# Kernel tuning notes

Measured on AMD Instinct MI355X. Metric: run time of the kernel, lower is better.

Reference implementation:

```python
import jax, jax.numpy as jnp
import numpy as np

B, C, D, J = 8, 2048, 128, 128

def setup_inputs() -> dict:
    key = jax.random.key(0)
    ks = jax.random.split(key, 24)
    s = 0.02
    inp = {
        "operation_features": jax.random.normal(ks[0], (B, C, D), jnp.float32),
        "relations": jax.random.randint(ks[1], (B, C - 2, 2), 0, C, jnp.int64),
        "begins_idx": jax.random.randint(ks[2], (B, J), 0, C, jnp.int64),
        "ends_idx": jax.random.randint(ks[3], (B, J), 0, C, jnp.int64),
        "same_type_mask": (jax.random.uniform(ks[4], (B, C, C)) > 0.5).astype(jnp.float32),
        # BeginEndEncoder
        "W_begin": jax.random.normal(ks[5], (D, D), jnp.float32) * s,
        "b_begin": jnp.zeros((D,), jnp.float32),
        "W_end": jax.random.normal(ks[6], (D, D), jnp.float32) * s,
        "b_end": jnp.zeros((D,), jnp.float32),
        # OperationTimeRelationEncoder.mix: Linear(3D -> D)
        "W_mix3": jax.random.normal(ks[7], (3 * D, D), jnp.float32) * s,
        "b_mix3": jnp.zeros((D,), jnp.float32),
        # SelfAttention (hidden_dim = D)
        "W_qkv": jax.random.normal(ks[8], (D, 3 * D), jnp.float32) * s,
        "b_qkv": jnp.zeros((3 * D,), jnp.float32),
        "w_score": jax.random.normal(ks[9], (2 * D,), jnp.float32) * s,
        "b_score": jnp.zeros((), jnp.float32),
        "W_out": jax.random.normal(ks[10], (D, D), jnp.float32) * s,
        "b_out": jnp.zeros((D,), jnp.float32),
        # block mix: Linear(2D -> D)
        "W_mix2": jax.random.normal(ks[11], (2 * D, D), jnp.float32) * s,
        "b_mix2": jnp.zeros((D,), jnp.float32),
    }
    return inp

def _gather_ops(ops, idx):
    # ops: [B,C,D], idx: [B,M] -> [B,M,D]  (torch.gather along dim 1 with expanded index)
    Bb, _, Dd = ops.shape
    M = idx.shape[1]
    return jnp.take_along_axis(ops, jnp.broadcast_to(idx[:, :, None], (Bb, M, Dd)), axis=1)

def reference(operation_features, relations, begins_idx, ends_idx, same_type_mask,
              W_begin, b_begin, W_end, b_end, W_mix3, b_mix3,
              W_qkv, b_qkv, w_score, b_score, W_out, b_out, W_mix2, b_mix2):
    ops = operation_features
    Dd = ops.shape[-1]
    # --- OperationTimeRelationEncoder ---
    pred = _gather_ops(ops, relations[..., 0])      # [B,C-2,D]
    succ = _gather_ops(ops, relations[..., 1])      # [B,C-2,D]
    concated = jnp.concatenate([ops[:, :-2, :], pred, succ], axis=-1)  # [B,C-2,3D]
    mixed = concated @ W_mix3 + b_mix3              # [B,C-2,D]
    begin_f = _gather_ops(ops, begins_idx) @ W_begin + b_begin  # [B,J,D]
    end_f = _gather_ops(ops, ends_idx) @ W_end + b_end
    begin = jnp.mean(begin_f, axis=1)               # [B,D]
    end = jnp.mean(end_f, axis=1)
    seq = jnp.concatenate([mixed, begin[:, None, :], end[:, None, :]], axis=1)  # [B,C,D]
    # --- SelfAttention (GAT-style additive score, decomposed to avoid CxCx2h blowup) ---
    qkv = ops @ W_qkv + b_qkv                       # [B,C,3D]
    q, k, v = jnp.split(qkv, 3, axis=-1)
    sq = q @ w_score[:Dd]                           # [B,C]  q_i . w_q
    sk = k @ w_score[Dd:]                           # [B,C]  k_j . w_k
    scores = jax.nn.leaky_relu(sq[:, :, None] + sk[:, None, :] + b_score)  # [B,C,C]
    attn = jax.nn.softmax(scores * same_type_mask, axis=-1)                # multiplicative mask, as in torch
    weighted = jnp.einsum('bij,bjd->bid', attn, v)  # [B,C,D]
    same_type = weighted @ W_out + b_out            # [B,C,D]
    # --- final mix ---
    return jnp.concatenate([seq, same_type], axis=-1) @ W_mix2 + b_mix2  # [B,C,D]
```

## Files before the change

kernel.cpp:

```cpp
#include <hip/hip_runtime.h>
#include <cstddef>

typedef __bf16 bf16;
typedef __bf16 bf16x4 __attribute__((ext_vector_type(4)));
typedef __bf16 bf16x8 __attribute__((ext_vector_type(8)));
typedef float  f32x4  __attribute__((ext_vector_type(4)));

#define MFMA16(a, b, c) __builtin_amdgcn_mfma_f32_16x16x32_bf16((a), (b), (c), 0, 0, 0)

#define BB 8
#define CC 2048
#define DD 128
#define JJN 128

#define WS_PK    ((size_t)0)
#define WS_OPS16 ((size_t)8388608)
#define WS_SQF   ((size_t)12582912)
#define WS_SKF   ((size_t)12648448)
#define WS_G1T   ((size_t)12713984)
#define WS_G2T   ((size_t)12746752)
#define WS_G3T   ((size_t)12779520)
#define WS_WCT   ((size_t)12812288)
#define WS_GBT   ((size_t)12845056)
#define WS_GET   ((size_t)12877824)
#define WS_UQK   ((size_t)12910592)
#define WS_BBM   ((size_t)12911104)
#define WS_BBB   ((size_t)12911616)
#define WS_BBE   ((size_t)12912128)
#define WS_SC    ((size_t)12912640)
#define WS_WCN   ((size_t)12913152)
#define WS_GBN   ((size_t)12945920)
#define WS_GEN   ((size_t)12978688)
#define WS_MEANV ((size_t)17205760)

__global__ __launch_bounds__(256) void k_prepcast(
    const float* __restrict__ ops, bf16* __restrict__ ops16,
    const int* __restrict__ begins, const int* __restrict__ ends,
    const float* __restrict__ Wmix3, const float* __restrict__ Wmix2,
    const float* __restrict__ Wout,  const float* __restrict__ Wbegin,
    const float* __restrict__ Wend,  const float* __restrict__ Wqkv,
    const float* __restrict__ bqkv,  const float* __restrict__ wscore,
    const float* __restrict__ bscore,const float* __restrict__ bmix3,
    const float* __restrict__ bout,  const float* __restrict__ bmix2,
    const float* __restrict__ bbegin,const float* __restrict__ bend,
    bf16* __restrict__ G1T, bf16* __restrict__ G2T, bf16* __restrict__ G3T,
    bf16* __restrict__ WCT, bf16* __restrict__ GBT, bf16* __restrict__ GET,
    bf16* __restrict__ WCN, bf16* __restrict__ GBN, bf16* __restrict__ GEN,
    bf16* __restrict__ uqk, float* __restrict__ BBM, float* __restrict__ BBB,
    float* __restrict__ BBE, float* __restrict__ sc, float* __restrict__ MEANV)
{
    __shared__ bf16  LshT[128 * 132];
    __shared__ float Rsh[128 * 8];
    int wg = blockIdx.x;
    int t  = threadIdx.x;

    if (wg == 0) {
        for (int half = 0; half < 2; ++half) {
            #pragma unroll
            for (int pass = 0; pass < 16; ++pass) {
                int idx = pass * 256 + t;
                int d   = idx >> 5;
                int e0  = (idx & 31) * 4;
                f32x4 v = *(const f32x4*)(Wqkv + d*384 + half*128 + e0);
                #pragma unroll
                for (int jj = 0; jj < 4; ++jj)
                    LshT[(e0 + jj)*132 + d] = (bf16)v[jj];
            }
            if (t < 32) {
                f32x4 wv = *(const f32x4*)(wscore + half*128 + t*4);
                #pragma unroll
                for (int jj = 0; jj < 4; ++jj) Rsh[t*4 + jj] = wv[jj];
            }
            __syncthreads();
            if (t < 128) {
                float s = 0.f;
                for (int e = 0; e < 128; ++e)
                    s += (float)LshT[e*132 + t] * Rsh[e];
                uqk[half*128 + t] = (bf16)s;
            }
            __syncthreads();
        }
        float bm = 0.f, bb_ = 0.f, be_ = 0.f, bon = 0.f;
        for (int half = 0; half < 2; ++half) {
            #pragma unroll
            for (int pass = 0; pass < 16; ++pass) {
                int idx = pass * 256 + t;
                int f   = idx >> 5;
                int e0  = (idx & 31) * 4;
                f32x4 v = *(const f32x4*)(Wmix2 + (size_t)(half*128 + f)*128 + e0);
                #pragma unroll
                for (int jj = 0; jj < 4; ++jj)
                    LshT[f*132 + e0 + jj] = (bf16)v[jj];
            }
            if (t < 32) {
                if (half == 0) {
                    f32x4 v0 = *(const f32x4*)(bmix3  + t*4);
                    f32x4 v1 = *(const f32x4*)(bbegin + t*4);
                    f32x4 v2 = *(const f32x4*)(bend   + t*4);
                    #pragma unroll
                    for (int jj = 0; jj < 4; ++jj) {
                        Rsh[t*4 + jj]       = v0[jj];
                        Rsh[128 + t*4 + jj] = v1[jj];
                        Rsh[256 + t*4 + jj] = v2[jj];
                    }
                } else {
                    f32x4 v3 = *(const f32x4*)(bout + t*4);
                    #pragma unroll
                    for (int jj = 0; jj < 4; ++jj) Rsh[t*4 + jj] = v3[jj];
                }
            }
            __syncthreads();
            if (t < 128) {
                if (half == 0) {
                    for (int f = 0; f < 128; ++f) {
                        float wv = (float)LshT[f*132 + t];
                        bm  += Rsh[f]       * wv;
                        bb_ += Rsh[128 + f] * wv;
                        be_ += Rsh[256 + f] * wv;
                    }
                } else {
                    for (int f = 0; f < 128; ++f)
                        bon += Rsh[f] * (float)LshT[f*132 + t];
                }
            }
            __syncthreads();
        }
        if (t < 128) {
            float bm2 = bmix2[t];
            BBM[t] = bm  + bon + bm2;
            BBB[t] = bb_ + bon + bm2;
            BBE[t] = be_ + bon + bm2;
        }
        if (t >= 128) {
            int e2 = t - 128;
            Rsh[512 + e2] = bqkv[e2]       * wscore[e2];
            Rsh[640 + e2] = bqkv[128 + e2] * wscore[128 + e2];
        }
        __syncthreads();
        if (t == 0) {
            float cq = 0.f, ck = 0.f;
            for (int e2 = 0; e2 < 128; ++e2) {
                cq += Rsh[512 + e2];
                ck += Rsh[640 + e2];
            }
            sc[0] = cq + bscore[0];
            sc[1] = ck;
        }
        return;
    }
    if (wg <= 16) {
        int task = wg - 1;
        int b2 = task >> 1, which = task & 1;
        const int* idxp = which ? (ends + b2 * JJN) : (begins + b2 * JJN);
        int* ish = (int*)Rsh;
        if (t < JJN) ish[t] = idxp[t];
        __syncthreads();
        int d = t & 127, half = t >> 7;
        const float* opsb = ops + (size_t)b2 * CC * DD;
        float s = 0.f;
        #pragma unroll 8
        for (int j = 0; j < 64; ++j) {
            int r = ish[half * 64 + j];
            s += opsb[(size_t)r * DD + d];
        }
        float* fsh = Rsh + 256;
        fsh[half * 128 + d] = s;
        __syncthreads();
        if (t < 128)
            MEANV[task * 128 + t] = (fsh[t] + fsh[128 + t]) * (1.0f / (float)JJN);
        return;
    }
    if (wg <= 112) {
        int id  = wg - 17;
        int mat = id >> 4, sub = id & 15;
        const float* L; const float* R; bf16* O; bf16* O2;
        switch (mat) {
            case 0: L = Wmix3;           R = Wmix2;           O = G1T; O2 = nullptr; break;
            case 1: L = Wmix3 + 128*128; R = Wmix2;           O = G2T; O2 = nullptr; break;
            case 2: L = Wmix3 + 256*128; R = Wmix2;           O = G3T; O2 = nullptr; break;
            case 3: L = Wout;            R = Wmix2 + 128*128; O = WCT; O2 = WCN; break;
            case 4: L = Wbegin;          R = Wmix2;           O = GBT; O2 = GBN; break;
            default:L = Wend;            R = Wmix2;           O = GET; O2 = GEN; break;
        }
        int e0 = sub * 8;
        #pragma unroll
        for (int pass = 0; pass < 16; ++pass) {
            int idx = pass * 256 + t;
            int d   = idx >> 5;
            int f0  = (idx & 31) * 4;
            f32x4 v = *(const f32x4*)(L + d * 128 + f0);
            #pragma unroll
            for (int jj = 0; jj < 4; ++jj)
                LshT[(f0 + jj) * 132 + d] = (bf16)v[jj];
        }
        #pragma unroll
        for (int pass = 0; pass < 4; ++pass) {
            int idx = pass * 256 + t;
            int f   = idx >> 3;
            int ee  = idx & 7;
            Rsh[f * 8 + ee] = R[f * 128 + e0 + ee];
        }
        __syncthreads();
        int ee = t >> 5;
        int e  = e0 + ee;
        int d0 = (t & 31) * 4;
        float s[4] = {0.f, 0.f, 0.f, 0.f};
        for (int f = 0; f < 128; ++f) {
            bf16x4 lv = *(const bf16x4*)&LshT[f * 132 + d0];
            float rv = Rsh[f * 8 + ee];
            #pragma unroll
            for (int dd = 0; dd < 4; ++dd)
                s[dd] += (float)lv[dd] * rv;
        }
        #pragma unroll
        for (int dd = 0; dd < 4; ++dd) {
            O[e * 128 + d0 + dd] = (bf16)s[dd];
            if (O2) O2[(d0 + dd) * 128 + e] = (bf16)s[dd];
        }
        return;
    }
    size_t i = (size_t)(wg - 113) * 256 + t;
    f32x4 a = *(const f32x4*)(ops + i * 8);
    f32x4 b = *(const f32x4*)(ops + i * 8 + 4);
    bf16x8 o;
    #pragma unroll
    for (int e = 0; e < 4; ++e) { o[e] = (bf16)a[e]; o[4 + e] = (bf16)b[e]; }
    *(bf16x8*)(ops16 + i * 8) = o;
}

__global__ __launch_bounds__(256) void k_v(
    const bf16* __restrict__ ops16, const float* __restrict__ Wqkv,
    const float* __restrict__ bqkv, const bf16* __restrict__ uqk,
    const float* __restrict__ sc,
    bf16* __restrict__ PK, float* __restrict__ sqf, float* __restrict__ skf)
{
    __shared__ bf16 A[144 * 136];
    int b  = blockIdx.x >> 4;
    int jt = (blockIdx.x & 15) * 128;
    int t  = threadIdx.x;
    #pragma unroll
    for (int pass = 0; pass < 16; ++pass) {
        int idx = pass * 256 + t;
        int d   = idx >> 5;
        int n0  = (idx & 31) * 4;
        f32x4 v = *(const f32x4*)(Wqkv + d*384 + 256 + n0);
        #pragma unroll
        for (int jj = 0; jj < 4; ++jj)
            A[(n0 + jj)*136 + d] = (bf16)v[jj];
    }
    {
        int row = t >> 7, col = t & 127;
        A[(128 + row)*136 + col] = uqk[row*128 + col];
    }
    for (int idx = t; idx < 14*136; idx += 256)
        A[130*136 + idx] = (bf16)0.f;
    __syncthreads();

    int lane = t & 63, w = t >> 6;
    int m = lane & 15, q = lane >> 4;
    f32x4 acc[9][2];
    #pragma unroll
    for (int rb = 0; rb < 9; ++rb)
        #pragma unroll
        for (int cb = 0; cb < 2; ++cb)
            acc[rb][cb] = {0.f, 0.f, 0.f, 0.f};

    const bf16* opsb = ops16 + (size_t)b * CC * DD;
    #pragma unroll
    for (int kc = 0; kc < 4; ++kc) {
        bf16x8 bfr[2];
        #pragma unroll
        for (int cb = 0; cb < 2; ++cb) {
            int j = jt + w*32 + cb*16 + m;
            bfr[cb] = *(const bf16x8*)(opsb + (size_t)j*DD + kc*32 + q*8);
        }
        #pragma unroll
        for (int rb = 0; rb < 9; ++rb) {
            bf16x8 afr = *(const bf16x8*)&A[(rb*16 + m)*136 + kc*32 + q*8];
            acc[rb][0] = MFMA16(afr, bfr[0], acc[rb][0]);
            acc[rb][1] = MFMA16(afr, bfr[1], acc[rb][1]);
        }
    }
    float cqb = sc[0], ckv = sc[1];
    #pragma unroll
    for (int cb = 0; cb < 2; ++cb) {
        int j = jt + w*32 + cb*16 + m;
        if (q == 0) {
            sqf[b*CC + j] = acc[8][cb][0] + cqb;
            skf[b*CC + j] = acc[8][cb][1] + ckv;
        }
    }
    __syncthreads();
    bf16* pack = A;
    #pragma unroll
    for (int cb = 0; cb < 2; ++cb) {
        int qq_base = cb*2 + (m>>3);
        int e       = m & 7;
        #pragma unroll
        for (int rb = 0; rb < 8; ++rb) {
            #pragma unroll
            for (int r = 0; r < 4; ++r) {
                float v = acc[rb][cb][r] + bqkv[256 + rb*16 + q*4 + r];
                pack[w*4096 + rb*512 + qq_base*128 + (q*4+r)*8 + e] = (bf16)v;
            }
        }
    }
    __syncthreads();
    bf16* pkb = PK + (size_t)b * DD * CC + (size_t)jt * 128;
    #pragma unroll
    for (int pass = 0; pass < 8; ++pass) {
        int lidx = pass * 256 + t;
        *(uint4*)(pkb + (size_t)lidx * 8) = *(const uint4*)&pack[lidx * 8];
    }
}

struct MaskLd { f32x4 v[8]; };

__device__ __forceinline__ MaskLd stage_load(const float* __restrict__ mrow0,
                                             int st, int lane)
{
    MaskLd L;
    int rr0 = lane >> 4, cc = (lane & 15) * 4;
    const float* src = mrow0 + st * 64 + cc;
    #pragma unroll
    for (int k = 0; k < 8; ++k)
        L.v[k] = __builtin_nontemporal_load(
            (const f32x4*)(src + ((size_t)(rr0 + k * 4)) * CC));
    return L;
}

__device__ __forceinline__ void stage_write(const MaskLd& L, bf16* mb,
                                            int buf, int lane)
{
    int rr0 = lane >> 4, cc = (lane & 15) * 4;
    bf16* dst = mb + buf * 2816;
    #pragma unroll
    for (int k = 0; k < 8; ++k) {
        bf16x4 o;
        #pragma unroll
        for (int e = 0; e < 4; ++e) o[e] = (bf16)L.v[k][e];
        *(bf16x4*)(dst + (rr0 + k * 4) * 88 + cc) = o;
    }
}

__device__ __forceinline__ void load_vb(const bf16* __restrict__ pkb, int jc,
                                        int q, int m, bf16x8 vb[8])
{
    #pragma unroll
    for (int nb = 0; nb < 8; ++nb)
        vb[nb] = *(const bf16x8*)(pkb + ((size_t)(((jc*8 + nb)*4 + q)*16 + m)) * 8);
}

__device__ __forceinline__ void substep(const bf16* mb, const float* skb,
    int buf, int st, int sub, int tile, int q, int m, float sq,
    const bf16x8 vb[8], float& lsum, f32x4 acc[8])
{
    bf16x8 mk = *(const bf16x8*)(mb + buf * 2816 + (tile*16 + m) * 88
                                 + sub * 32 + q * 8);
    int jo = st * 64 + sub * 32 + q * 8;
    f32x4 s0 = *(const f32x4*)(skb + jo);
    f32x4 s1 = *(const f32x4*)(skb + jo + 4);
    float sks[8] = {s0[0], s0[1], s0[2], s0[3], s1[0], s1[1], s1[2], s1[3]};
    bf16x8 a;
    #pragma unroll
    for (int e = 0; e < 8; ++e) {
        float tv = sq + sks[e];
        float lr = fmaxf(tv, 0.01f * tv);
        float z  = lr * (float)mk[e];
        float p  = __expf(z);
        lsum += p;
        a[e] = (bf16)p;
    }
    #pragma unroll
    for (int nb = 0; nb < 8; ++nb)
        acc[nb] = MFMA16(a, vb[nb], acc[nb]);
}

__global__ __launch_bounds__(256) void k_attepi(
    const float* __restrict__ mask, const bf16* __restrict__ PK,
    const float* __restrict__ sqf, const float* __restrict__ skf,
    const bf16* __restrict__ ops16, const int* __restrict__ relations,
    const bf16* __restrict__ G1T, const bf16* __restrict__ G2T,
    const bf16* __restrict__ G3T, const bf16* __restrict__ WCT,
    const bf16* __restrict__ GBN, const bf16* __restrict__ GEN,
    const bf16* __restrict__ WCN,
    const float* __restrict__ BBM, const float* __restrict__ BBB,
    const float* __restrict__ BBE, const float* __restrict__ MEANV,
    float* __restrict__ out)
{
    __shared__ __align__(16) char smem[53248];
    int t    = threadIdx.x;
    int lane = t & 63, w = t >> 6;
    int b    = blockIdx.x & 7;
    int i0   = (blockIdx.x >> 3) << 5;
    int m = lane & 15, q = lane >> 4;

    bf16*  mbuf = (bf16*)(smem + w * 11264);
    float* skb  = (float*)(smem + 45056 + w * 2048);

    {
        const float* src = skf + b*CC + w*512;
        f32x4 v0 = *(const f32x4*)(src + lane*4);
        f32x4 v1 = *(const f32x4*)(src + 256 + lane*4);
        *(f32x4*)(skb + lane*4) = v0;
        *(f32x4*)(skb + 256 + lane*4) = v1;
    }
    float sq0 = sqf[b*CC + i0 + m];
    float sq1 = sqf[b*CC + i0 + 16 + m];
    const float* mrow0 = mask + ((size_t)(b*CC + i0))*CC + w*512;
    const bf16*  pkb   = PK + (size_t)b * DD * CC;
    int jc0 = w * 16;

    f32x4 acc0[8], acc1[8];
    #pragma unroll
    for (int nb = 0; nb < 8; ++nb) {
        acc0[nb] = {0.f, 0.f, 0.f, 0.f};
        acc1[nb] = {0.f, 0.f, 0.f, 0.f};
    }
    float lsum0 = 0.f, lsum1 = 0.f;

    {   MaskLd r0 = stage_load(mrow0, 0, lane);
        stage_write(r0, mbuf, 0, lane); }
    MaskLd r1 = stage_load(mrow0, 1, lane);
    MaskLd r2 = stage_load(mrow0, 2, lane);

    int buf = 0;
    for (int st = 0; st < 8; ++st) {
        #pragma unroll
        for (int sub = 0; sub < 2; ++sub) {
            bf16x8 vb[8];
            load_vb(pkb, jc0 + st*2 + sub, q, m, vb);
            substep(mbuf, skb, buf, st, sub, 0, q, m, sq0, vb, lsum0, acc0);
            substep(mbuf, skb, buf, st, sub, 1, q, m, sq1, vb, lsum1, acc1);
        }
        if (st + 1 < 8) stage_write(r1, mbuf, buf ^ 1, lane);
        r1 = r2;
        if (st + 3 < 8) r2 = stage_load(mrow0, st + 3, lane);
        buf ^= 1;
    }

    __syncthreads();
    float* Osh  = (float*)smem;
    float* Lsh  = (float*)(smem + 33792);
    bf16*  Obuf = (bf16*)(smem + 43520);
    #pragma unroll
    for (int tile = 0; tile < 2; ++tile) {
        float ls = tile ? lsum1 : lsum0;
        ls += __shfl_xor(ls, 16, 64);
        ls += __shfl_xor(ls, 32, 64);
        if (q == 0) Lsh[w * 16 + m] = ls;
        const f32x4* acc = tile ? acc1 : acc0;
        #pragma unroll
        for (int nb = 0; nb < 8; ++nb)
            #pragma unroll
            for (int r = 0; r < 4; ++r)
                Osh[(w * 16 + q * 4 + r) * 132 + nb * 16 + m] = acc[nb][r];
        __syncthreads();

        int r   = t >> 4;
        int c0e = (t & 15) * 8;
        float l = Lsh[r] + Lsh[16 + r] + Lsh[32 + r] + Lsh[48 + r];
        float inv = 1.0f / l;
        bf16x8 o;
        #pragma unroll
        for (int e = 0; e < 8; ++e) {
            float s = Osh[r * 132 + c0e + e] + Osh[(16 + r) * 132 + c0e + e]
                    + Osh[(32 + r) * 132 + c0e + e] + Osh[(48 + r) * 132 + c0e + e];
            o[e] = (bf16)(s * inv);
        }
        *(bf16x8*)&Obuf[(tile * 16 + r) * 136 + c0e] = o;
        __syncthreads();
    }

    bf16* Abuf = (bf16*)smem;
    bf16* Bbuf = (bf16*)(smem + 8704);

    f32x4 eacc[2][2];
    #pragma unroll
    for (int rb = 0; rb < 2; ++rb)
        #pragma unroll
        for (int cb = 0; cb < 2; ++cb)
            eacc[rb][cb] = {0.f, 0.f, 0.f, 0.f};

    const bf16* Bsrc[4] = {G1T, G2T, G3T, WCT};
    int arow = t >> 3, ao = (t & 7) * 16;
    int brow = t >> 1, bo2 = (t & 1) * 64;
    int c = i0 + arow;

    for (int term = 0; term < 4; ++term) {
        if (term < 3) {
            const bf16* src;
            if (term == 0) src = ops16 + ((size_t)(b * CC + c)) * DD;
            else {
                int ridx = relations[((size_t)b * (CC - 2) + min(c, CC - 3)) * 2 + (term - 1)];
                src = ops16 + ((size_t)(b * CC) + ridx) * DD;
            }
            *(uint4*)&Abuf[arow * 136 + ao]     = *(const uint4*)(src + ao);
            *(uint4*)&Abuf[arow * 136 + ao + 8] = *(const uint4*)(src + ao + 8);
        }
        const uint4* bs = (const uint4*)(Bsrc[term] + brow * 128 + bo2);
        uint4* bd = (uint4*)&Bbuf[brow * 136 + bo2];
        #pragma unroll
        for (int ii = 0; ii < 8; ++ii) bd[ii] = bs[ii];
        __syncthreads();

        const bf16* Asrc = (term == 3) ? Obuf : Abuf;
        #pragma unroll
        for (int kc = 0; kc < 4; ++kc) {
            bf16x8 bfr[2];
            #pragma unroll
            for (int cb = 0; cb < 2; ++cb)
                bfr[cb] = *(const bf16x8*)&Bbuf[(w * 32 + cb * 16 + m) * 136 + kc * 32 + q * 8];
            #pragma unroll
            for (int rb = 0; rb < 2; ++rb) {
                bf16x8 afr = *(const bf16x8*)&Asrc[(rb * 16 + m) * 136 + kc * 32 + q * 8];
                eacc[rb][0] = MFMA16(afr, bfr[0], eacc[rb][0]);
                eacc[rb][1] = MFMA16(afr, bfr[1], eacc[rb][1]);
            }
        }
        __syncthreads();
    }
    #pragma unroll
    for (int cb = 0; cb < 2; ++cb) {
        int col = w * 32 + cb * 16 + m;
        float bias = BBM[col];
        #pragma unroll
        for (int rb = 0; rb < 2; ++rb) {
            #pragma unroll
            for (int r = 0; r < 4; ++r) {
                int cg = i0 + rb * 16 + q * 4 + r;
                if (cg < CC - 2)
                    out[((size_t)(b * CC) + cg) * DD + col] = eacc[rb][cb][r] + bias;
            }
        }
    }

    if (i0 == CC - 32) {
        __syncthreads();
        float* mv2 = (float*)smem;
        int grp = t >> 7, tl = t & 127;
        mv2[grp * 128 + tl] = MEANV[((size_t)b * 2 + grp) * 128 + tl];
        __syncthreads();
        int which = grp;
        const bf16* G    = which ? GEN : GBN;
        const float* Bv  = which ? BBE : BBB;
        const bf16* orow = Obuf + (30 + which) * 136;
        float a = Bv[tl];
        const float* mv = mv2 + grp * 128;
        for (int d = 0; d < 128; ++d) {
            a += mv[d] * (float)G[d * 128 + tl];
            a += (float)orow[d] * (float)WCN[d * 128 + tl];
        }
        out[((size_t)b * CC + (CC - 2 + which)) * DD + tl] = a;
    }
}

extern "C" void kernel_launch(void* const* d_in, const int* in_sizes, int n_in,
                              void* d_out, int out_size, void* d_ws, size_t ws_size,
                              hipStream_t stream)
{
    const float* ops      = (const float*)d_in[0];
    const int*  relations = (const int*)d_in[1];
    const int*  begins    = (const int*)d_in[2];
    const int*  ends      = (const int*)d_in[3];
    const float* mask     = (const float*)d_in[4];
    const float* Wbegin   = (const float*)d_in[5];
    const float* bbegin   = (const float*)d_in[6];
    const float* Wend     = (const float*)d_in[7];
    const float* bend     = (const float*)d_in[8];
    const float* Wmix3    = (const float*)d_in[9];
    const float* bmix3    = (const float*)d_in[10];
    const float* Wqkv     = (const float*)d_in[11];
    const float* bqkv     = (const float*)d_in[12];
    const float* wscore   = (const float*)d_in[13];
    const float* bscore   = (const float*)d_in[14];
    const float* Wout     = (const float*)d_in[15];
    const float* bout     = (const float*)d_in[16];
    const float* Wmix2    = (const float*)d_in[17];
    const float* bmix2    = (const float*)d_in[18];
    float* outp = (float*)d_out;

    char* ws = (char*)d_ws;
    bf16*  PK    = (bf16*)(ws + WS_PK);
    bf16*  OPS16 = (bf16*)(ws + WS_OPS16);
    float* sqf   = (float*)(ws + WS_SQF);
    float* skf   = (float*)(ws + WS_SKF);
    bf16*  G1T   = (bf16*)(ws + WS_G1T);
    bf16*  G2T   = (bf16*)(ws + WS_G2T);
    bf16*  G3T   = (bf16*)(ws + WS_G3T);
    bf16*  WCT   = (bf16*)(ws + WS_WCT);
    bf16*  GBT   = (bf16*)(ws + WS_GBT);
    bf16*  GET   = (bf16*)(ws + WS_GET);
    bf16*  WCN   = (bf16*)(ws + WS_WCN);
    bf16*  GBN   = (bf16*)(ws + WS_GBN);
    bf16*  GEN   = (bf16*)(ws + WS_GEN);
    bf16*  UQK   = (bf16*)(ws + WS_UQK);
    float* BBM   = (float*)(ws + WS_BBM);
    float* BBB   = (float*)(ws + WS_BBB);
    float* BBE   = (float*)(ws + WS_BBE);
    float* SC    = (float*)(ws + WS_SC);
    float* MEANV = (float*)(ws + WS_MEANV);

    k_prepcast<<<dim3(1137), dim3(256), 0, stream>>>(
        ops, OPS16, begins, ends,
        Wmix3, Wmix2, Wout, Wbegin, Wend, Wqkv, bqkv, wscore, bscore,
        bmix3, bout, bmix2, bbegin, bend,
        G1T, G2T, G3T, WCT, GBT, GET, WCN, GBN, GEN,
        UQK, BBM, BBB, BBE, SC, MEANV);

    k_v<<<dim3(128), dim3(256), 0, stream>>>(
        OPS16, Wqkv, bqkv, UQK, SC, PK, sqf, skf);

    k_attepi<<<dim3(512), dim3(256), 0, stream>>>(
        mask, PK, sqf, skf, OPS16, relations,
        G1T, G2T, G3T, WCT, GBN, GEN, WCN, BBM, BBB, BBE, MEANV, outp);
}
```

Before: 283.8 us.

## Double wave count in attention kernel and load mask directly to registers

The attention-epilogue kernel now runs 512 threads (8 waves) per block, so each wave covers 256 key columns instead of 512. Each wave reads mask values straight from global memory into registers in MFMA fragment layout, replacing the shared-memory staging buffer and its bf16 conversion. Partial outputs from the two wave halves are combined in shared memory with an added accumulate pass and extra barriers. The V/score projection kernel also moves to 256 blocks of 64 rows to raise occupancy. The direct mask loads use a strided per-lane access pattern instead of the earlier coalesced non-temporal loads.

```diff
diff --git a/kernel.cpp b/kernel.cpp
--- a/kernel.cpp
+++ b/kernel.cpp
@@ -235,8 +235,8 @@
     bf16* __restrict__ PK, float* __restrict__ sqf, float* __restrict__ skf)
 {
     __shared__ bf16 A[144 * 136];
-    int b  = blockIdx.x >> 4;
-    int jt = (blockIdx.x & 15) * 128;
+    int b  = blockIdx.x >> 5;
+    int jt = (blockIdx.x & 31) * 64;
     int t  = threadIdx.x;
     #pragma unroll
     for (int pass = 0; pass < 16; ++pass) {
@@ -258,89 +258,61 @@
 
     int lane = t & 63, w = t >> 6;
     int m = lane & 15, q = lane >> 4;
-    f32x4 acc[9][2];
-    #pragma unroll
-    for (int rb = 0; rb < 9; ++rb)
-        #pragma unroll
-        for (int cb = 0; cb < 2; ++cb)
-            acc[rb][cb] = {0.f, 0.f, 0.f, 0.f};
+    f32x4 acc[9];
+    #pragma unroll
+    for (int rb = 0; rb < 9; ++rb) acc[rb] = {0.f, 0.f, 0.f, 0.f};
 
     const bf16* opsb = ops16 + (size_t)b * CC * DD;
+    int j = jt + w*16 + m;
     #pragma unroll
     for (int kc = 0; kc < 4; ++kc) {
-        bf16x8 bfr[2];
-        #pragma unroll
-        for (int cb = 0; cb < 2; ++cb) {
-            int j = jt + w*32 + cb*16 + m;
-            bfr[cb] = *(const bf16x8*)(opsb + (size_t)j*DD + kc*32 + q*8);
-        }
+        bf16x8 bfr = *(const bf16x8*)(opsb + (size_t)j*DD + kc*32 + q*8);
         #pragma unroll
         for (int rb = 0; rb < 9; ++rb) {
             bf16x8 afr = *(const bf16x8*)&A[(rb*16 + m)*136 + kc*32 + q*8];
-            acc[rb][0] = MFMA16(afr, bfr[0], acc[rb][0]);
-            acc[rb][1] = MFMA16(afr, bfr[1], acc[rb][1]);
+            acc[rb] = MFMA16(afr, bfr, acc[rb]);
         }
     }
     float cqb = sc[0], ckv = sc[1];
-    #pragma unroll
-    for (int cb = 0; cb < 2; ++cb) {
-        int j = jt + w*32 + cb*16 + m;
-        if (q == 0) {
-            sqf[b*CC + j] = acc[8][cb][0] + cqb;
-            skf[b*CC + j] = acc[8][cb][1] + ckv;
-        }
+    if (q == 0) {
+        sqf[b*CC + j] = acc[8][0] + cqb;
+        skf[b*CC + j] = acc[8][1] + ckv;
     }
     __syncthreads();
     bf16* pack = A;
-    #pragma unroll
-    for (int cb = 0; cb < 2; ++cb) {
-        int qq_base = cb*2 + (m>>3);
-        int e       = m & 7;
+    {
+        int jcl = w >> 1;
+        int qv  = (w & 1) * 2 + (m >> 3);
+        int ev  = m & 7;
         #pragma unroll
         for (int rb = 0; rb < 8; ++rb) {
             #pragma unroll
             for (int r = 0; r < 4; ++r) {
-                float v = acc[rb][cb][r] + bqkv[256 + rb*16 + q*4 + r];
-                pack[w*4096 + rb*512 + qq_base*128 + (q*4+r)*8 + e] = (bf16)v;
+                float v = acc[rb][r] + bqkv[256 + rb*16 + q*4 + r];
+                pack[jcl*4096 + rb*512 + qv*128 + (q*4+r)*8 + ev] = (bf16)v;
             }
         }
     }
     __syncthreads();
     bf16* pkb = PK + (size_t)b * DD * CC + (size_t)jt * 128;
     #pragma unroll
-    for (int pass = 0; pass < 8; ++pass) {
+    for (int pass = 0; pass < 4; ++pass) {
         int lidx = pass * 256 + t;
         *(uint4*)(pkb + (size_t)lidx * 8) = *(const uint4*)&pack[lidx * 8];
     }
 }
 
-struct MaskLd { f32x4 v[8]; };
-
-__device__ __forceinline__ MaskLd stage_load(const float* __restrict__ mrow0,
-                                             int st, int lane)
-{
-    MaskLd L;
-    int rr0 = lane >> 4, cc = (lane & 15) * 4;
-    const float* src = mrow0 + st * 64 + cc;
-    #pragma unroll
-    for (int k = 0; k < 8; ++k)
-        L.v[k] = __builtin_nontemporal_load(
-            (const f32x4*)(src + ((size_t)(rr0 + k * 4)) * CC));
-    return L;
-}
-
-__device__ __forceinline__ void stage_write(const MaskLd& L, bf16* mb,
-                                            int buf, int lane)
-{
-    int rr0 = lane >> 4, cc = (lane & 15) * 4;
-    bf16* dst = mb + buf * 2816;
-    #pragma unroll
-    for (int k = 0; k < 8; ++k) {
-        bf16x4 o;
-        #pragma unroll
-        for (int e = 0; e < 4; ++e) o[e] = (bf16)L.v[k][e];
-        *(bf16x4*)(dst + (rr0 + k * 4) * 88 + cc) = o;
-    }
+struct MFrag { f32x4 a0, a1, b0, b1; };
+
+__device__ __forceinline__ MFrag mload(const float* __restrict__ r0,
+                                       const float* __restrict__ r1, int off)
+{
+    MFrag f;
+    f.a0 = *(const f32x4*)(r0 + off);
+    f.a1 = *(const f32x4*)(r0 + off + 4);
+    f.b0 = *(const f32x4*)(r1 + off);
+    f.b1 = *(const f32x4*)(r1 + off + 4);
+    return f;
 }
 
 __device__ __forceinline__ void load_vb(const bf16* __restrict__ pkb, int jc,
@@ -351,32 +323,34 @@
         vb[nb] = *(const bf16x8*)(pkb + ((size_t)(((jc*8 + nb)*4 + q)*16 + m)) * 8);
 }
 
-__device__ __forceinline__ void substep(const bf16* mb, const float* skb,
-    int buf, int st, int sub, int tile, int q, int m, float sq,
-    const bf16x8 vb[8], float& lsum, f32x4 acc[8])
-{
-    bf16x8 mk = *(const bf16x8*)(mb + buf * 2816 + (tile*16 + m) * 88
-                                 + sub * 32 + q * 8);
-    int jo = st * 64 + sub * 32 + q * 8;
-    f32x4 s0 = *(const f32x4*)(skb + jo);
-    f32x4 s1 = *(const f32x4*)(skb + jo + 4);
-    float sks[8] = {s0[0], s0[1], s0[2], s0[3], s1[0], s1[1], s1[2], s1[3]};
+__device__ __forceinline__ void substep2(const float* __restrict__ skw, int jo,
+    float sq, f32x4 m0, f32x4 m1, const bf16x8 vb[8], float& lsum, f32x4 acc[8])
+{
+    f32x4 s0 = *(const f32x4*)(skw + jo);
+    f32x4 s1 = *(const f32x4*)(skw + jo + 4);
     bf16x8 a;
     #pragma unroll
-    for (int e = 0; e < 8; ++e) {
-        float tv = sq + sks[e];
+    for (int e = 0; e < 4; ++e) {
+        float tv = sq + s0[e];
         float lr = fmaxf(tv, 0.01f * tv);
-        float z  = lr * (float)mk[e];
-        float p  = __expf(z);
+        float p  = __expf(lr * m0[e]);
         lsum += p;
         a[e] = (bf16)p;
     }
     #pragma unroll
+    for (int e = 0; e < 4; ++e) {
+        float tv = sq + s1[e];
+        float lr = fmaxf(tv, 0.01f * tv);
+        float p  = __expf(lr * m1[e]);
+        lsum += p;
+        a[4 + e] = (bf16)p;
+    }
+    #pragma unroll
     for (int nb = 0; nb < 8; ++nb)
         acc[nb] = MFMA16(a, vb[nb], acc[nb]);
 }
 
-__global__ __launch_bounds__(256) void k_attepi(
+__global__ __launch_bounds__(512) void k_attepi(
     const float* __restrict__ mask, const bf16* __restrict__ PK,
     const float* __restrict__ sqf, const float* __restrict__ skf,
     const bf16* __restrict__ ops16, const int* __restrict__ relations,
@@ -388,28 +362,23 @@
     const float* __restrict__ BBE, const float* __restrict__ MEANV,
     float* __restrict__ out)
 {
-    __shared__ __align__(16) char smem[53248];
+    __shared__ __align__(16) char smem[52224];
     int t    = threadIdx.x;
     int lane = t & 63, w = t >> 6;
     int b    = blockIdx.x & 7;
     int i0   = (blockIdx.x >> 3) << 5;
     int m = lane & 15, q = lane >> 4;
 
-    bf16*  mbuf = (bf16*)(smem + w * 11264);
-    float* skb  = (float*)(smem + 45056 + w * 2048);
-
-    {
-        const float* src = skf + b*CC + w*512;
-        f32x4 v0 = *(const f32x4*)(src + lane*4);
-        f32x4 v1 = *(const f32x4*)(src + 256 + lane*4);
-        *(f32x4*)(skb + lane*4) = v0;
-        *(f32x4*)(skb + 256 + lane*4) = v1;
-    }
+    float* skb = (float*)smem;
+    float* skw = skb + w * 256;
+    *(f32x4*)(skw + lane * 4) = *(const f32x4*)(skf + b*CC + w*256 + lane*4);
+
     float sq0 = sqf[b*CC + i0 + m];
     float sq1 = sqf[b*CC + i0 + 16 + m];
-    const float* mrow0 = mask + ((size_t)(b*CC + i0))*CC + w*512;
-    const bf16*  pkb   = PK + (size_t)b * DD * CC;
-    int jc0 = w * 16;
+    const float* mr0 = mask + ((size_t)(b*CC + i0 + m))*CC + w*256 + q*8;
+    const float* mr1 = mr0 + (size_t)16 * CC;
+    const bf16*  pkb = PK + (size_t)b * DD * CC;
+    int jc0 = w * 8;
 
     f32x4 acc0[8], acc1[8];
     #pragma unroll
@@ -419,72 +388,75 @@
     }
     float lsum0 = 0.f, lsum1 = 0.f;
 
-    {   MaskLd r0 = stage_load(mrow0, 0, lane);
-        stage_write(r0, mbuf, 0, lane); }
-    MaskLd r1 = stage_load(mrow0, 1, lane);
-    MaskLd r2 = stage_load(mrow0, 2, lane);
-
-    int buf = 0;
-    for (int st = 0; st < 8; ++st) {
-        #pragma unroll
-        for (int sub = 0; sub < 2; ++sub) {
-            bf16x8 vb[8];
-            load_vb(pkb, jc0 + st*2 + sub, q, m, vb);
-            substep(mbuf, skb, buf, st, sub, 0, q, m, sq0, vb, lsum0, acc0);
-            substep(mbuf, skb, buf, st, sub, 1, q, m, sq1, vb, lsum1, acc1);
-        }
-        if (st + 1 < 8) stage_write(r1, mbuf, buf ^ 1, lane);
-        r1 = r2;
-        if (st + 3 < 8) r2 = stage_load(mrow0, st + 3, lane);
-        buf ^= 1;
-    }
-
-    __syncthreads();
-    float* Osh  = (float*)smem;
-    float* Lsh  = (float*)(smem + 33792);
+    MFrag mA = mload(mr0, mr1, 0);
+    #pragma unroll
+    for (int s = 0; s < 8; s += 2) {
+        MFrag mB = mload(mr0, mr1, (s + 1) * 32);
+        bf16x8 v[8];
+        load_vb(pkb, jc0 + s, q, m, v);
+        substep2(skw, s*32 + q*8, sq0, mA.a0, mA.a1, v, lsum0, acc0);
+        substep2(skw, s*32 + q*8, sq1, mA.b0, mA.b1, v, lsum1, acc1);
+        if (s + 2 < 8) mA = mload(mr0, mr1, (s + 2) * 32);
+        load_vb(pkb, jc0 + s + 1, q, m, v);
+        substep2(skw, (s+1)*32 + q*8, sq0, mB.a0, mB.a1, v, lsum0, acc0);
+        substep2(skw, (s+1)*32 + q*8, sq1, mB.b0, mB.b1, v, lsum1, acc1);
+    }
+
+    float* Osh  = (float*)(smem + 8704);
+    float* Lsh  = (float*)(smem + 42496);
     bf16*  Obuf = (bf16*)(smem + 43520);
+
     #pragma unroll
     for (int tile = 0; tile < 2; ++tile) {
         float ls = tile ? lsum1 : lsum0;
         ls += __shfl_xor(ls, 16, 64);
         ls += __shfl_xor(ls, 32, 64);
-        if (q == 0) Lsh[w * 16 + m] = ls;
         const f32x4* acc = tile ? acc1 : acc0;
-        #pragma unroll
-        for (int nb = 0; nb < 8; ++nb)
-            #pragma unroll
-            for (int r = 0; r < 4; ++r)
-                Osh[(w * 16 + q * 4 + r) * 132 + nb * 16 + m] = acc[nb][r];
-        __syncthreads();
-
-        int r   = t >> 4;
-        int c0e = (t & 15) * 8;
-        float l = Lsh[r] + Lsh[16 + r] + Lsh[32 + r] + Lsh[48 + r];
-        float inv = 1.0f / l;
-        bf16x8 o;
-        #pragma unroll
-        for (int e = 0; e < 8; ++e) {
-            float s = Osh[r * 132 + c0e + e] + Osh[(16 + r) * 132 + c0e + e]
-                    + Osh[(32 + r) * 132 + c0e + e] + Osh[(48 + r) * 132 + c0e + e];
-            o[e] = (bf16)(s * inv);
-        }
-        *(bf16x8*)&Obuf[(tile * 16 + r) * 136 + c0e] = o;
+        if (w < 4) {
+            if (q == 0) Lsh[w*16 + m] = ls;
+            #pragma unroll
+            for (int nb = 0; nb < 8; ++nb)
+                #pragma unroll
+                for (int r = 0; r < 4; ++r)
+                    Osh[(w*16 + q*4 + r)*132 + nb*16 + m] = acc[nb][r];
+        }
+        __syncthreads();
+        if (w >= 4) {
+            if (q == 0) Lsh[(w-4)*16 + m] += ls;
+            #pragma unroll
+            for (int nb = 0; nb < 8; ++nb)
+                #pragma unroll
+                for (int r = 0; r < 4; ++r)
+                    Osh[((w-4)*16 + q*4 + r)*132 + nb*16 + m] += acc[nb][r];
+        }
+        __syncthreads();
+        if (t < 256) {
+            int r   = t >> 4;
+            int c0e = (t & 15) * 8;
+            float l = Lsh[r] + Lsh[16 + r] + Lsh[32 + r] + Lsh[48 + r];
+            float inv = 1.0f / l;
+            bf16x8 o;
+            #pragma unroll
+            for (int e = 0; e < 8; ++e) {
+                float s = Osh[r*132 + c0e + e] + Osh[(16 + r)*132 + c0e + e]
+                        + Osh[(32 + r)*132 + c0e + e] + Osh[(48 + r)*132 + c0e + e];
+                o[e] = (bf16)(s * inv);
+            }
+            *(bf16x8*)&Obuf[(tile * 16 + r) * 136 + c0e] = o;
+        }
         __syncthreads();
     }
 
     bf16* Abuf = (bf16*)smem;
     bf16* Bbuf = (bf16*)(smem + 8704);
 
-    f32x4 eacc[2][2];
-    #pragma unroll
-    for (int rb = 0; rb < 2; ++rb)
-        #pragma unroll
-        for (int cb = 0; cb < 2; ++cb)
-            eacc[rb][cb] = {0.f, 0.f, 0.f, 0.f};
+    f32x4 eacc[2];
+    eacc[0] = {0.f, 0.f, 0.f, 0.f};
+    eacc[1] = {0.f, 0.f, 0.f, 0.f};
 
     const bf16* Bsrc[4] = {G1T, G2T, G3T, WCT};
-    int arow = t >> 3, ao = (t & 7) * 16;
-    int brow = t >> 1, bo2 = (t & 1) * 64;
+    int arow = t >> 4, ao = (t & 15) * 8;
+    int brow = t >> 2, bo2 = (t & 3) * 32;
     int c = i0 + arow;
 
     for (int term = 0; term < 4; ++term) {
@@ -495,42 +467,36 @@
                 int ridx = relations[((size_t)b * (CC - 2) + min(c, CC - 3)) * 2 + (term - 1)];
                 src = ops16 + ((size_t)(b * CC) + ridx) * DD;
             }
-            *(uint4*)&Abuf[arow * 136 + ao]     = *(const uint4*)(src + ao);
-            *(uint4*)&Abuf[arow * 136 + ao + 8] = *(const uint4*)(src + ao + 8);
-        }
-        const uint4* bs = (const uint4*)(Bsrc[term] + brow * 128 + bo2);
-        uint4* bd = (uint4*)&Bbuf[brow * 136 + bo2];
-        #pragma unroll
-        for (int ii = 0; ii < 8; ++ii) bd[ii] = bs[ii];
+            *(uint4*)&Abuf[arow * 136 + ao] = *(const uint4*)(src + ao);
+        }
+        #pragma unroll
+        for (int ii = 0; ii < 4; ++ii)
+            *(uint4*)&Bbuf[brow * 136 + bo2 + ii*8] =
+                *(const uint4*)(Bsrc[term] + brow * 128 + bo2 + ii*8);
         __syncthreads();
 
         const bf16* Asrc = (term == 3) ? Obuf : Abuf;
         #pragma unroll
         for (int kc = 0; kc < 4; ++kc) {
-            bf16x8 bfr[2];
-            #pragma unroll
-            for (int cb = 0; cb < 2; ++cb)
-                bfr[cb] = *(const bf16x8*)&Bbuf[(w * 32 + cb * 16 + m) * 136 + kc * 32 + q * 8];
+            bf16x8 bfr = *(const bf16x8*)&Bbuf[(w*16 + m)*136 + kc*32 + q*8];
             #pragma unroll
             for (int rb = 0; rb < 2; ++rb) {
-                bf16x8 afr = *(const bf16x8*)&Asrc[(rb * 16 + m) * 136 + kc * 32 + q * 8];
-                eacc[rb][0] = MFMA16(afr, bfr[0], eacc[rb][0]);
-                eacc[rb][1] = MFMA16(afr, bfr[1], eacc[rb][1]);
-            }
-        }
-        __syncthreads();
-    }
-    #pragma unroll
-    for (int cb = 0; cb < 2; ++cb) {
-        int col = w * 32 + cb * 16 + m;
+                bf16x8 afr = *(const bf16x8*)&Asrc[(rb*16 + m)*136 + kc*32 + q*8];
+                eacc[rb] = MFMA16(afr, bfr, eacc[rb]);
+            }
+        }
+        __syncthreads();
+    }
+    {
+        int col = w*16 + m;
         float bias = BBM[col];
         #pragma unroll
         for (int rb = 0; rb < 2; ++rb) {
             #pragma unroll
             for (int r = 0; r < 4; ++r) {
-                int cg = i0 + rb * 16 + q * 4 + r;
+                int cg = i0 + rb*16 + q*4 + r;
                 if (cg < CC - 2)
-                    out[((size_t)(b * CC) + cg) * DD + col] = eacc[rb][cb][r] + bias;
+                    out[((size_t)(b * CC) + cg) * DD + col] = eacc[rb][r] + bias;
             }
         }
     }
@@ -538,20 +504,24 @@
     if (i0 == CC - 32) {
         __syncthreads();
         float* mv2 = (float*)smem;
-        int grp = t >> 7, tl = t & 127;
-        mv2[grp * 128 + tl] = MEANV[((size_t)b * 2 + grp) * 128 + tl];
-        __syncthreads();
-        int which = grp;
-        const bf16* G    = which ? GEN : GBN;
-        const float* Bv  = which ? BBE : BBB;
-        const bf16* orow = Obuf + (30 + which) * 136;
-        float a = Bv[tl];
-        const float* mv = mv2 + grp * 128;
-        for (int d = 0; d < 128; ++d) {
-            a += mv[d] * (float)G[d * 128 + tl];
-            a += (float)orow[d] * (float)WCN[d * 128 + tl];
-        }
-        out[((size_t)b * CC + (CC - 2 + which)) * DD + tl] = a;
+        if (t < 256)
+            mv2[(t >> 7) * 128 + (t & 127)] =
+                MEANV[((size_t)b * 2 + (t >> 7)) * 128 + (t & 127)];
+        __syncthreads();
+        if (t < 256) {
+            int grp = t >> 7, tl = t & 127;
+            int which = grp;
+            const bf16* G    = which ? GEN : GBN;
+            const float* Bv  = which ? BBE : BBB;
+            const bf16* orow = Obuf + (30 + which) * 136;
+            float a = Bv[tl];
+            const float* mv = mv2 + grp * 128;
+            for (int d = 0; d < 128; ++d) {
+                a += mv[d] * (float)G[d * 128 + tl];
+                a += (float)orow[d] * (float)WCN[d * 128 + tl];
+            }
+            out[((size_t)b * CC + (CC - 2 + which)) * DD + tl] = a;
+        }
     }
 }
 
@@ -608,10 +578,10 @@
         G1T, G2T, G3T, WCT, GBT, GET, WCN, GBN, GEN,
         UQK, BBM, BBB, BBE, SC, MEANV);
 
-    k_v<<<dim3(128), dim3(256), 0, stream>>>(
+    k_v<<<dim3(256), dim3(256), 0, stream>>>(
         OPS16, Wqkv, bqkv, UQK, SC, PK, sqf, skf);
 
-    k_attepi<<<dim3(512), dim3(256), 0, stream>>>(
+    k_attepi<<<dim3(512), dim3(512), 0, stream>>>(
         mask, PK, sqf, skf, OPS16, relations,
         G1T, G2T, G3T, WCT, GBN, GEN, WCN, BBM, BBB, BBE, MEANV, outp);
 }
```

Result: no change. 286.8 us (+1.1%).
